# Kernel optimization log

Measured on AMD Instinct MI355X. Metric: run time of the kernel, lower is better.

## Reference

```python
import jax, jax.numpy as jnp
import numpy as np

BETA = 0.05
KNN = 6
UL_ALPHA = 0.05
UL_BETA = 1.0


def setup_inputs() -> dict:
    key = jax.random.key(0)
    k1, k2, k3 = jax.random.split(key, 3)
    B, D, N = 256, 2048, 16384
    inputs = jax.random.normal(k1, (B, D), dtype=jnp.float32)
    em = jax.random.normal(k2, (N, D), dtype=jnp.float32)
    # exemplar memory rows are kept unit-norm by the update rule
    em = em / jnp.linalg.norm(em, axis=1, keepdims=True)
    targets = jax.random.randint(k3, (B,), 0, N, dtype=jnp.int64)
    return {"inputs": inputs, "em": em, "targets": targets, "epoch": 10}


def smooth_hot(logits, targets, em, k):
    # Vectorized k-reciprocal neighbor search (replaces the per-sample Python loop).
    m, n = logits.shape
    # index_sorted[:, :k] == top-k class indices per sample
    _, topk_idx = jax.lax.top_k(logits, k)            # [m, k]
    neigh = em[topk_idx]                               # [m, k, d]
    sims = jnp.einsum('mkd,nd->mkn', neigh, em)        # [m, k, n]
    _, neigh_topk = jax.lax.top_k(sims, k)             # [m, k, k]
    # neighbor j of sample i is reciprocal if anchor (top-1 of i) is in its top-k
    anchor = topk_idx[:, :1, None]                     # [m, 1, 1]
    recip = (neigh_topk == anchor).any(axis=-1)        # [m, k]
    weights = jnp.where(recip, 3.0 / k, 0.0).astype(logits.dtype)
    rows = jnp.arange(m)[:, None]
    onehot = jnp.zeros_like(logits).at[rows, topk_idx].set(weights)
    onehot = onehot.at[jnp.arange(m), targets].set(1.0)
    return onehot


def reference(inputs, em, targets, epoch):
    # ExemplarMemory.forward: similarity logits against the memory bank
    logits = (inputs @ em.T) / BETA                    # [B, N]
    # epoch >= 5 and knn > 0 branch (epoch=10)
    onehot = jax.lax.stop_gradient(
        smooth_hot(jax.lax.stop_gradient(logits), targets, em, KNN))
    logp = jax.nn.log_softmax(logits, axis=1)
    beta_loss = (-(onehot * logp).sum(axis=1)).mean()
    t_re = jnp.where(onehot == 0.0, jnp.float32(1e-4), onehot)
    alpha_loss = (-(jax.nn.softmax(logits, axis=1) * jnp.log(t_re)).sum(axis=1)).mean()
    return (UL_ALPHA * alpha_loss, UL_BETA * beta_loss)
```

## Files before the change

kernel.cpp:

```cpp
#include <hip/hip_runtime.h>
#include <math.h>

#define DIMK 2048
#define NEMB 16384
#define NB 256
#define NR2 1536
#define INV_BETA 20.0f
#define NEG_INF (-3.0e38f)

typedef short short8 __attribute__((ext_vector_type(8)));
typedef float f32x4 __attribute__((ext_vector_type(4)));
typedef const __attribute__((address_space(1))) unsigned int* gas_ptr;
typedef __attribute__((address_space(3))) unsigned int* las_ptr;

__device__ __forceinline__ void gl_lds16(const void* g, void* l) {
  __builtin_amdgcn_global_load_lds((gas_ptr)g, (las_ptr)l, 16, 0, 0);
}

__device__ __forceinline__ unsigned short f2bf(float f) {
  unsigned u = __float_as_uint(f);
  u += 0x7fffu + ((u >> 16) & 1u);
  return (unsigned short)(u >> 16);
}

__device__ __forceinline__ void ins6i(float x, int xi, float v[6], int vi[6]) {
  if (x > v[5] || (x == v[5] && xi < vi[5])) {
    v[5] = x; vi[5] = xi;
#pragma unroll
    for (int j = 5; j > 0; j--) {
      if (v[j] > v[j - 1] || (v[j] == v[j - 1] && vi[j] < vi[j - 1])) {
        float tv = v[j]; v[j] = v[j - 1]; v[j - 1] = tv;
        int ti = vi[j]; vi[j] = vi[j - 1]; vi[j - 1] = ti;
      }
    }
  }
}

__global__ __launch_bounds__(256) void cvt_kernel(const float* __restrict__ src,
                                                  unsigned short* __restrict__ dst, int n4) {
  int i = blockIdx.x * 256 + threadIdx.x;
  if (i < n4) {
    float4 f = ((const float4*)src)[i];
    ushort4 o;
    o.x = f2bf(f.x); o.y = f2bf(f.y); o.z = f2bf(f.z); o.w = f2bf(f.w);
    ((ushort4*)dst)[i] = o;
  }
}

template <int MODE>
__global__ __launch_bounds__(256, 4) void gemm_kernel(
    const unsigned short* __restrict__ Abase, const unsigned short* __restrict__ Bbase,
    const int* __restrict__ nidx, float* __restrict__ outC,
    const float* __restrict__ saIn, int* __restrict__ cntOut) {
  constexpr int MTILE = (MODE == 0) ? 64 : 128;
  constexpr int MI = 4;
  constexpr int NI = (MODE == 0) ? 2 : 4;
  constexpr int NSUB_A = MTILE / 16;
  constexpr int NSUB = NSUB_A + 8;
  constexpr int NA = NSUB / 4;
  constexpr int NK = DIMK / 32;

  __shared__ unsigned short st[2][NSUB * 512];
  __shared__ int rowIdxSh[128];
  __shared__ float saSh[128];
  __shared__ int cntSh[128];
  int t = threadIdx.x;
  int lane = t & 63, wave = t >> 6;
  int quad = lane >> 4, l16 = lane & 15;
  int wr = (MODE == 0) ? 0 : (wave >> 1);
  int wc = (MODE == 0) ? wave : (wave & 1);
  int bn = blockIdx.x, bm = blockIdx.y;

  if constexpr (MODE == 1) {
    if (t < 128) {
      rowIdxSh[t] = nidx[bm * 128 + t];
      saSh[t] = saIn[bm * 128 + t];
      cntSh[t] = 0;
    }
  }
  __syncthreads();

  const unsigned short* agp[NA];
  int soff[NA];
  {
    int seg = lane >> 4;
#pragma unroll
    for (int a = 0; a < NA; a++) {
      int s = wave + a * 4;
      const unsigned short* basep;
      size_t goff;
      if (s < NSUB_A) {
        int r = s * 16 + l16;
        int grow = (MODE == 0) ? (bm * MTILE + r) : rowIdxSh[r];
        basep = Abase;
        goff = (size_t)grow * DIMK;
      } else {
        int r = (s - NSUB_A) * 16 + l16;
        basep = Bbase;
        goff = (size_t)(bn * 128 + r) * DIMK;
      }
      agp[a] = basep + goff + seg * 8;
      soff[a] = s * 512;
    }
  }

  f32x4 acc[MI][NI];
#pragma unroll
  for (int mi = 0; mi < MI; mi++)
#pragma unroll
    for (int ni = 0; ni < NI; ni++) acc[mi][ni] = (f32x4)0.0f;

  int lo = lane * 8;

#pragma unroll
  for (int a = 0; a < NA; a++) gl_lds16(agp[a], &st[0][soff[a]]);
  __syncthreads();

  for (int k = 0; k < NK; k++) {
    int cur = k & 1, nxt = cur ^ 1;
    if (k + 1 < NK) {
#pragma unroll
      for (int a = 0; a < NA; a++) gl_lds16(agp[a] + (k + 1) * 32, &st[nxt][soff[a]]);
    }
    const unsigned short* hb = &st[cur][0];
    short8 af[MI], bfv[NI];
#pragma unroll
    for (int mi = 0; mi < MI; mi++)
      af[mi] = *(const short8*)&hb[(wr * MI + mi) * 512 + lo];
#pragma unroll
    for (int ni = 0; ni < NI; ni++)
      bfv[ni] = *(const short8*)&hb[(NSUB_A + wc * NI + ni) * 512 + lo];
#pragma unroll
    for (int mi = 0; mi < MI; mi++)
#pragma unroll
      for (int ni = 0; ni < NI; ni++)
        acc[mi][ni] =
            __builtin_amdgcn_mfma_f32_16x16x32_bf16(af[mi], bfv[ni], acc[mi][ni], 0, 0, 0);
    __syncthreads();
  }

  if constexpr (MODE == 0) {
#pragma unroll
    for (int mi = 0; mi < MI; mi++) {
      int row = bm * MTILE + mi * 16 + quad * 4;
#pragma unroll
      for (int ni = 0; ni < NI; ni++) {
        int col = bn * 128 + wave * 32 + ni * 16 + l16;
#pragma unroll
        for (int rr = 0; rr < 4; rr++)
          outC[(size_t)(row + rr) * NEMB + col] = acc[mi][ni][rr] * INV_BETA;
      }
    }
  } else {
#pragma unroll
    for (int mi = 0; mi < MI; mi++) {
#pragma unroll
      for (int rr = 0; rr < 4; rr++) {
        int rloc = wr * 64 + mi * 16 + quad * 4 + rr;
        float s = saSh[rloc];
        int c = 0;
#pragma unroll
        for (int ni = 0; ni < NI; ni++) c += (acc[mi][ni][rr] > s) ? 1 : 0;
        c += __shfl_xor(c, 1, 64);
        c += __shfl_xor(c, 2, 64);
        c += __shfl_xor(c, 4, 64);
        c += __shfl_xor(c, 8, 64);
        if (l16 == 0) atomicAdd(&cntSh[rloc], c);
      }
    }
    __syncthreads();
    if (t < 128) atomicAdd(&cntOut[bm * 128 + t], cntSh[t]);
  }
}

__global__ __launch_bounds__(1024) void rowstats_kernel(
    const float* __restrict__ logits, float* __restrict__ topv,
    int* __restrict__ topi, float* __restrict__ lse) {
  int m = blockIdx.x, t = threadIdx.x;
  const float4* row4 = (const float4*)(logits + (size_t)m * NEMB);
  float v6[6]; int i6[6];
#pragma unroll
  for (int j = 0; j < 6; j++) { v6[j] = NEG_INF; i6[j] = 0x7fffffff; }
  float vals[16];
#pragma unroll
  for (int j = 0; j < 4; j++) {
    float4 f = row4[t + j * 1024];
    vals[j * 4 + 0] = f.x; vals[j * 4 + 1] = f.y;
    vals[j * 4 + 2] = f.z; vals[j * 4 + 3] = f.w;
  }
  float mx = vals[0];
#pragma unroll
  for (int r = 1; r < 16; r++) mx = fmaxf(mx, vals[r]);
  float sme = 0.f;
#pragma unroll
  for (int r = 0; r < 16; r++) sme += expf(vals[r] - mx);
#pragma unroll
  for (int j = 0; j < 4; j++) {
    int base = (t + j * 1024) * 4;
#pragma unroll
    for (int b = 0; b < 4; b++) ins6i(vals[j * 4 + b], base + b, v6, i6);
  }
  __shared__ float sv[1024 * 6]; __shared__ int si[1024 * 6];
  __shared__ float smx[1024], ssm[1024];
#pragma unroll
  for (int j = 0; j < 6; j++) { sv[t * 6 + j] = v6[j]; si[t * 6 + j] = i6[j]; }
  smx[t] = mx; ssm[t] = sme;
  __syncthreads();
  for (int s = 512; s > 0; s >>= 1) {
    if (t < s) {
      float mo = smx[t + s], lo = ssm[t + s];
      float mn = fmaxf(smx[t], mo);
      ssm[t] = ssm[t] * expf(smx[t] - mn) + lo * expf(mo - mn);
      smx[t] = mn;
#pragma unroll
      for (int j = 0; j < 6; j++) ins6i(sv[(t + s) * 6 + j], si[(t + s) * 6 + j], v6, i6);
#pragma unroll
      for (int j = 0; j < 6; j++) { sv[t * 6 + j] = v6[j]; si[t * 6 + j] = i6[j]; }
    }
    __syncthreads();
  }
  if (t == 0) {
    lse[m] = smx[0] + logf(ssm[0]);
#pragma unroll
    for (int j = 0; j < 6; j++) { topv[m * 6 + j] = v6[j]; topi[m * 6 + j] = i6[j]; }
  }
}

__global__ __launch_bounds__(256) void sa_kernel(const float* __restrict__ em,
                                                 const int* __restrict__ topi,
                                                 float* __restrict__ sa,
                                                 int* __restrict__ cnt) {
  int gid = blockIdx.x * 256 + threadIdx.x;
  int w = gid >> 6, lane = gid & 63;
  if (w >= NR2) return;
  if (lane == 1) cnt[w] = 0;
  int m = w / 6;
  int i = topi[w], a = topi[m * 6];
  const float* ei = em + (size_t)i * DIMK;
  const float* ea = em + (size_t)a * DIMK;
  float s = 0.f;
  for (int d = lane; d < DIMK; d += 64) s += ei[d] * ea[d];
#pragma unroll
  for (int off = 32; off > 0; off >>= 1) s += __shfl_down(s, off, 64);
  if (lane == 0) sa[w] = s;
}

__global__ __launch_bounds__(256) void final_kernel(
    const float* __restrict__ logits, const float* __restrict__ topv,
    const int* __restrict__ topi, const float* __restrict__ lse_arr,
    const int* __restrict__ cnt, const int* __restrict__ targets,
    float* __restrict__ out) {
  int m = threadIdx.x;
  float lse = lse_arr[m];
  int tgt = targets[m];
  float tl = logits[(size_t)m * NEMB + tgt];
  float beta = 0.f, Ps = 0.f, nbp = 0.f;
  bool tin = false;
#pragma unroll
  for (int k = 0; k < 6; k++) {
    int idx = topi[m * 6 + k]; float v = topv[m * 6 + k];
    float p = expf(v - lse);
    if (idx == tgt) { tin = true; beta += (lse - v); Ps += p; }
    else if (cnt[m * 6 + k] < 6) { beta += 0.5f * (lse - v); Ps += p; nbp += p; }
  }
  if (!tin) { beta += (lse - tl); Ps += expf(tl - lse); }
  float alpha = 9.2103404f * (1.f - Ps) + 0.6931472f * nbp;
  __shared__ float sA[256], sB2[256];
  sA[m] = alpha; sB2[m] = beta;
  __syncthreads();
  for (int s = 128; s > 0; s >>= 1) {
    if (m < s) { sA[m] += sA[m + s]; sB2[m] += sB2[m + s]; }
    __syncthreads();
  }
  if (m == 0) { out[0] = 0.05f * sA[0] / 256.f; out[1] = sB2[0] / 256.f; }
}

extern "C" void kernel_launch(void* const* d_in, const int* in_sizes, int n_in,
                              void* d_out, int out_size, void* d_ws, size_t ws_size,
                              hipStream_t stream) {
  const float* x = (const float*)d_in[0];
  const float* em = (const float*)d_in[1];
  const int* targets = (const int*)d_in[2];
  char* ws = (char*)d_ws;
  unsigned short* em_bf = (unsigned short*)ws;
  unsigned short* x_bf  = (unsigned short*)(ws + 67108864);
  float* logits = (float*)(ws + 68157440);
  int*   cnt    = (int*)  (ws + 84934656);
  float* topv   = (float*)(ws + 89653248);
  int*   topi   = (int*)  (ws + 89659392);
  float* lse    = (float*)(ws + 89665536);
  float* sa     = (float*)(ws + 89666560);

  cvt_kernel<<<dim3(32768), dim3(256), 0, stream>>>(em, em_bf, NEMB * DIMK / 4);
  cvt_kernel<<<dim3(512), dim3(256), 0, stream>>>(x, x_bf, NB * DIMK / 4);
  gemm_kernel<0><<<dim3(128, 4), dim3(256), 0, stream>>>(x_bf, em_bf, (const int*)nullptr,
                                                         logits, (const float*)nullptr,
                                                         (int*)nullptr);
  rowstats_kernel<<<dim3(256), dim3(1024), 0, stream>>>(logits, topv, topi, lse);
  sa_kernel<<<dim3(384), dim3(256), 0, stream>>>(em, topi, sa, cnt);
  gemm_kernel<1><<<dim3(128, 12), dim3(256), 0, stream>>>(em_bf, em_bf, topi,
                                                          (float*)nullptr, sa, cnt);
  final_kernel<<<dim3(1), dim3(256), 0, stream>>>(logits, topv, topi, lse, cnt, targets,
                                                  (float*)d_out);
}
```

Baseline: 487.8 us.

## Early-exit neighbor-count GEMM via survivor compaction and register-staged loads

```diff
diff --git a/kernel.cpp b/kernel.cpp
--- a/kernel.cpp
+++ b/kernel.cpp
@@ -10,12 +10,6 @@
 
 typedef short short8 __attribute__((ext_vector_type(8)));
 typedef float f32x4 __attribute__((ext_vector_type(4)));
-typedef const __attribute__((address_space(1))) unsigned int* gas_ptr;
-typedef __attribute__((address_space(3))) unsigned int* las_ptr;
-
-__device__ __forceinline__ void gl_lds16(const void* g, void* l) {
-  __builtin_amdgcn_global_load_lds((gas_ptr)g, (las_ptr)l, 16, 0, 0);
-}
 
 __device__ __forceinline__ unsigned short f2bf(float f) {
   unsigned u = __float_as_uint(f);
@@ -48,10 +42,11 @@
 }
 
 template <int MODE>
-__global__ __launch_bounds__(256, 4) void gemm_kernel(
+__global__ __launch_bounds__(256, 3) void gemm_rs(
     const unsigned short* __restrict__ Abase, const unsigned short* __restrict__ Bbase,
     const int* __restrict__ nidx, float* __restrict__ outC,
-    const float* __restrict__ saIn, int* __restrict__ cntOut) {
+    const float* __restrict__ saIn, int* __restrict__ cntOut,
+    const int* __restrict__ surv, const int* __restrict__ nsurvp) {
   constexpr int MTILE = (MODE == 0) ? 64 : 128;
   constexpr int MI = 4;
   constexpr int NI = (MODE == 0) ? 2 : 4;
@@ -64,21 +59,34 @@
   __shared__ int rowIdxSh[128];
   __shared__ float saSh[128];
   __shared__ int cntSh[128];
+  __shared__ int outRowSh[128];
   int t = threadIdx.x;
   int lane = t & 63, wave = t >> 6;
   int quad = lane >> 4, l16 = lane & 15;
   int wr = (MODE == 0) ? 0 : (wave >> 1);
   int wc = (MODE == 0) ? wave : (wave & 1);
   int bn = blockIdx.x, bm = blockIdx.y;
-
-  if constexpr (MODE == 1) {
+  int nvalid = 128;
+
+  if constexpr (MODE == 2) {
+    int ns = nsurvp[0];
+    if (bm * 128 >= ns) return;
+    nvalid = (ns - bm * 128 < 128) ? (ns - bm * 128) : 128;
+  }
+  if constexpr (MODE >= 1) {
     if (t < 128) {
-      rowIdxSh[t] = nidx[bm * 128 + t];
-      saSh[t] = saIn[bm * 128 + t];
+      int r;
+      if constexpr (MODE == 1) r = bm * 128 + t;
+      else r = surv[bm * 128 + ((t < nvalid) ? t : 0)];
+      rowIdxSh[t] = nidx[r];
+      saSh[t] = saIn[r];
       cntSh[t] = 0;
-    }
-  }
-  __syncthreads();
+      outRowSh[t] = r;
+    }
+    __syncthreads();
+  }
+
+  int colbase = (MODE == 2) ? ((bn + 16) * 128) : (bn * 128);
 
   const unsigned short* agp[NA];
   int soff[NA];
@@ -87,19 +95,17 @@
 #pragma unroll
     for (int a = 0; a < NA; a++) {
       int s = wave + a * 4;
+      size_t grow;
       const unsigned short* basep;
-      size_t goff;
       if (s < NSUB_A) {
         int r = s * 16 + l16;
-        int grow = (MODE == 0) ? (bm * MTILE + r) : rowIdxSh[r];
+        grow = (MODE == 0) ? (size_t)(bm * MTILE + r) : (size_t)rowIdxSh[r];
         basep = Abase;
-        goff = (size_t)grow * DIMK;
       } else {
-        int r = (s - NSUB_A) * 16 + l16;
+        grow = (size_t)(colbase + (s - NSUB_A) * 16 + l16);
         basep = Bbase;
-        goff = (size_t)(bn * 128 + r) * DIMK;
       }
-      agp[a] = basep + goff + seg * 8;
+      agp[a] = basep + grow * DIMK + seg * 8;
       soff[a] = s * 512;
     }
   }
@@ -112,17 +118,17 @@
 
   int lo = lane * 8;
 
-#pragma unroll
-  for (int a = 0; a < NA; a++) gl_lds16(agp[a], &st[0][soff[a]]);
-  __syncthreads();
-
-  for (int k = 0; k < NK; k++) {
-    int cur = k & 1, nxt = cur ^ 1;
-    if (k + 1 < NK) {
-#pragma unroll
-      for (int a = 0; a < NA; a++) gl_lds16(agp[a] + (k + 1) * 32, &st[nxt][soff[a]]);
-    }
-    const unsigned short* hb = &st[cur][0];
+  short8 rA[NA], rB2[NA];
+  auto LOADT = [&](short8* R, int kk) {
+#pragma unroll
+    for (int a = 0; a < NA; a++) R[a] = *(const short8*)(agp[a] + kk * 32);
+  };
+  auto WRITET = [&](const short8* R, int b) {
+#pragma unroll
+    for (int a = 0; a < NA; a++) *(short8*)&st[b][soff[a] + lo] = R[a];
+  };
+  auto COMPUTE = [&](int b) {
+    const unsigned short* hb = &st[b][0];
     short8 af[MI], bfv[NI];
 #pragma unroll
     for (int mi = 0; mi < MI; mi++)
@@ -136,6 +142,21 @@
       for (int ni = 0; ni < NI; ni++)
         acc[mi][ni] =
             __builtin_amdgcn_mfma_f32_16x16x32_bf16(af[mi], bfv[ni], acc[mi][ni], 0, 0, 0);
+  };
+
+  LOADT(rA, 0);
+  LOADT(rB2, 1);
+  WRITET(rA, 0);
+  __syncthreads();
+
+  for (int k = 0; k < NK; k += 2) {
+    if (k + 2 < NK) LOADT(rA, k + 2);
+    COMPUTE(0);
+    WRITET(rB2, 1);
+    __syncthreads();
+    if (k + 3 < NK) LOADT(rB2, k + 3);
+    COMPUTE(1);
+    if (k + 2 < NK) WRITET(rA, 0);
     __syncthreads();
   }
 
@@ -169,8 +190,24 @@
       }
     }
     __syncthreads();
-    if (t < 128) atomicAdd(&cntOut[bm * 128 + t], cntSh[t]);
-  }
+    if (t < nvalid) atomicAdd(&cntOut[outRowSh[t]], cntSh[t]);
+  }
+}
+
+__global__ __launch_bounds__(256) void compact_kernel(const int* __restrict__ cnt,
+                                                      int* __restrict__ surv,
+                                                      int* __restrict__ nsurv) {
+  __shared__ int ctr;
+  if (threadIdx.x == 0) ctr = 0;
+  __syncthreads();
+  for (int i = threadIdx.x; i < NR2; i += 256) {
+    if (cnt[i] < 6) {
+      int p = atomicAdd(&ctr, 1);
+      surv[p] = i;
+    }
+  }
+  __syncthreads();
+  if (threadIdx.x == 0) nsurv[0] = ctr;
 }
 
 __global__ __launch_bounds__(1024) void rowstats_kernel(
@@ -208,9 +245,9 @@
   __syncthreads();
   for (int s = 512; s > 0; s >>= 1) {
     if (t < s) {
-      float mo = smx[t + s], lo = ssm[t + s];
+      float mo = smx[t + s], lo2 = ssm[t + s];
       float mn = fmaxf(smx[t], mo);
-      ssm[t] = ssm[t] * expf(smx[t] - mn) + lo * expf(mo - mn);
+      ssm[t] = ssm[t] * expf(smx[t] - mn) + lo2 * expf(mo - mn);
       smx[t] = mn;
 #pragma unroll
       for (int j = 0; j < 6; j++) ins6i(sv[(t + s) * 6 + j], si[(t + s) * 6 + j], v6, i6);
@@ -286,6 +323,8 @@
   unsigned short* x_bf  = (unsigned short*)(ws + 67108864);
   float* logits = (float*)(ws + 68157440);
   int*   cnt    = (int*)  (ws + 84934656);
+  int*   surv   = (int*)  (ws + 84940800);
+  int*   nsurv  = (int*)  (ws + 84946944);
   float* topv   = (float*)(ws + 89653248);
   int*   topi   = (int*)  (ws + 89659392);
   float* lse    = (float*)(ws + 89665536);
@@ -293,13 +332,17 @@
 
   cvt_kernel<<<dim3(32768), dim3(256), 0, stream>>>(em, em_bf, NEMB * DIMK / 4);
   cvt_kernel<<<dim3(512), dim3(256), 0, stream>>>(x, x_bf, NB * DIMK / 4);
-  gemm_kernel<0><<<dim3(128, 4), dim3(256), 0, stream>>>(x_bf, em_bf, (const int*)nullptr,
-                                                         logits, (const float*)nullptr,
-                                                         (int*)nullptr);
+  gemm_rs<0><<<dim3(128, 4), dim3(256), 0, stream>>>(
+      x_bf, em_bf, (const int*)nullptr, logits, (const float*)nullptr, (int*)nullptr,
+      (const int*)nullptr, (const int*)nullptr);
   rowstats_kernel<<<dim3(256), dim3(1024), 0, stream>>>(logits, topv, topi, lse);
   sa_kernel<<<dim3(384), dim3(256), 0, stream>>>(em, topi, sa, cnt);
-  gemm_kernel<1><<<dim3(128, 12), dim3(256), 0, stream>>>(em_bf, em_bf, topi,
-                                                          (float*)nullptr, sa, cnt);
+  gemm_rs<1><<<dim3(16, 12), dim3(256), 0, stream>>>(
+      em_bf, em_bf, topi, (float*)nullptr, sa, cnt, (const int*)nullptr,
+      (const int*)nullptr);
+  compact_kernel<<<dim3(1), dim3(256), 0, stream>>>(cnt, surv, nsurv);
+  gemm_rs<2><<<dim3(112, 12), dim3(256), 0, stream>>>(
+      em_bf, em_bf, topi, (float*)nullptr, sa, cnt, surv, nsurv);
   final_kernel<<<dim3(1), dim3(256), 0, stream>>>(logits, topv, topi, lse, cnt, targets,
                                                   (float*)d_out);
 }
```

Measured after the change: 409.9 us. -16.0%, faster.
